# Optimization experiments

Measured on AMD Instinct MI355X. Metric: run time of the kernel, lower is better.

## Reference

```python
import jax, jax.numpy as jnp
import numpy as np

B, K, D = 4, 2048, 512
H, DQ, DV = 8, 64, 64
ATTN_SIZE = 128  # banded local window


def setup_inputs() -> dict:
    key = jax.random.key(0)
    ks = jax.random.split(key, 11)
    s = 1.0 / np.sqrt(D)
    so = 1.0 / np.sqrt(H * DV)
    return {
        "query": jax.random.normal(ks[0], (B, K, D), jnp.float32),
        "key": jax.random.normal(ks[1], (B, K, D), jnp.float32),
        "value": jax.random.normal(ks[2], (B, K, D), jnp.float32),
        "W_q": jax.random.uniform(ks[3], (H * DQ, D), jnp.float32, -s, s),
        "b_q": jax.random.uniform(ks[4], (H * DQ,), jnp.float32, -s, s),
        "W_k": jax.random.uniform(ks[5], (H * DQ, D), jnp.float32, -s, s),
        "b_k": jax.random.uniform(ks[6], (H * DQ,), jnp.float32, -s, s),
        "W_v": jax.random.uniform(ks[7], (H * DV, D), jnp.float32, -s, s),
        "b_v": jax.random.uniform(ks[8], (H * DV,), jnp.float32, -s, s),
        "W_o": jax.random.uniform(ks[9], (D, H * DV), jnp.float32, -so, so),
        "b_o": jax.random.uniform(ks[10], (D,), jnp.float32, -so, so),
    }


def reference(query, key, value, W_q, b_q, W_k, b_k, W_v, b_v, W_o, b_o):
    Klen = query.shape[1]
    # projections; chunk(h, -1) + cat(0) in torch == per-head split of last dim
    q = (query @ W_q.T + b_q).reshape(B, Klen, H, DQ)
    k = (key @ W_k.T + b_k).reshape(B, Klen, H, DQ)
    v = (value @ W_v.T + b_v).reshape(B, Klen, H, DV)
    # NOTE: original scales by sqrt(seq_len K), not sqrt(d_k)
    scores = jnp.einsum('bihq,bjhq->bhij', q, k) / jnp.sqrt(jnp.float32(Klen))
    i = jnp.arange(Klen)[:, None]
    j = jnp.arange(Klen)[None, :]
    # banded local mask (|i-j|<=attention_size) AND causal ('subsequent')
    allowed = (jnp.abs(i - j) <= ATTN_SIZE) & (j <= i)
    scores = jnp.where(allowed, scores, jnp.float32(-jnp.inf))
    probs = jax.nn.softmax(scores, axis=-1)
    attn = jnp.einsum('bhij,bjhv->bihv', probs, v).reshape(B, Klen, H * DV)
    return attn @ W_o.T + b_o
```

## Files before the change

### kernel.cpp

```cpp
#include <hip/hip_runtime.h>
#include <hip/hip_bf16.h>
#include <stdint.h>

#define B_ 4
#define K_ 2048
#define D_ 512
#define H_ 8
#define ATTN_ 128
#define M_ (B_ * K_)

typedef __attribute__((ext_vector_type(4))) float f32x4;
typedef __attribute__((ext_vector_type(8))) short bf16x8;
typedef __attribute__((ext_vector_type(8))) unsigned short u16x8;
typedef __attribute__((ext_vector_type(2))) unsigned int u32x2;

__device__ __forceinline__ unsigned short f2bf(float f) {
    union { float f; unsigned int i; } x; x.f = f;
    unsigned int r = x.i + 0x7fffu + ((x.i >> 16) & 1u);
    return (unsigned short)(r >> 16);
}
__device__ __forceinline__ float bf2f(unsigned short u) {
    union { unsigned int i; float f; } x; x.i = ((unsigned int)u) << 16; return x.f;
}
__device__ __forceinline__ void gload_lds16(const unsigned short* g, unsigned short* l) {
    __builtin_amdgcn_global_load_lds(
        (const __attribute__((address_space(1))) void*)g,
        (__attribute__((address_space(3))) void*)l, 16, 0, 0);
}
__device__ __forceinline__ unsigned lds_addr(const void* p) {
    return (unsigned)(unsigned long long)
        (const __attribute__((address_space(3))) void*)p;
}

struct Cvt { const float* s; unsigned short* d; int n8; };
struct CvtA { Cvt c[4]; };

__global__ __launch_bounds__(256)
void cvt_multi(CvtA a) {
    const Cvt c = a.c[blockIdx.y];
    const float4* s4 = (const float4*)c.s;
    u16x8* d8 = (u16x8*)c.d;
    for (int g = blockIdx.x * 256 + threadIdx.x; g < c.n8; g += gridDim.x * 256) {
        float4 f0 = s4[2 * g], f1 = s4[2 * g + 1];
        u16x8 o;
        o[0] = f2bf(f0.x); o[1] = f2bf(f0.y); o[2] = f2bf(f0.z); o[3] = f2bf(f0.w);
        o[4] = f2bf(f1.x); o[5] = f2bf(f1.y); o[6] = f2bf(f1.z); o[7] = f2bf(f1.w);
        d8[g] = o;
    }
}

struct QkvArgs {
    const float* A[3];
    const unsigned short* Wt[3];
    const float* bias[3];
    unsigned short* C[3];
};

__global__ __launch_bounds__(512, 4)
void gemm_qkv(QkvArgs args)
{
    __shared__ unsigned short As[2][128 * 64];
    __shared__ unsigned short Bs[2][128 * 64];

    const int z = blockIdx.y;
    const float* Az = args.A[z];
    const unsigned short* Wz = args.Wt[z];
    const float* biz = args.bias[z];
    unsigned short* Cz = args.C[z];

    const int id  = blockIdx.x;
    const int swz = (id & 7) * 32 + (id >> 3);
    const int bm  = (swz >> 2) * 128;
    const int bn  = (swz & 3) * 128;

    const int tid = threadIdx.x;
    const int w   = tid >> 6;
    const int l   = tid & 63;
    const int lr  = l & 15;
    const int lhi = l >> 4;
    const int wm  = (w >> 1) * 32;
    const int wn  = (w & 1) * 64;

    f32x4 acc[2][4];
    #pragma unroll
    for (int i = 0; i < 2; ++i)
        #pragma unroll
        for (int j = 0; j < 4; ++j) acc[i][j] = (f32x4){0.f, 0.f, 0.f, 0.f};

    float4 fa[2][2];
    auto loadA = [&](int t) {
        const int k0 = t * 64;
        #pragma unroll
        for (int it = 0; it < 2; ++it) {
            const int cid = it * 512 + tid;
            const int r = cid >> 3;
            const int c = (cid & 7) ^ (r & 7);
            const float* src = Az + (size_t)(bm + r) * D_ + k0 + c * 8;
            fa[it][0] = *(const float4*)src;
            fa[it][1] = *(const float4*)(src + 4);
        }
    };
    auto writeA = [&](int buf) {
        #pragma unroll
        for (int it = 0; it < 2; ++it) {
            const int cid = it * 512 + tid;
            u16x8 o;
            o[0] = f2bf(fa[it][0].x); o[1] = f2bf(fa[it][0].y);
            o[2] = f2bf(fa[it][0].z); o[3] = f2bf(fa[it][0].w);
            o[4] = f2bf(fa[it][1].x); o[5] = f2bf(fa[it][1].y);
            o[6] = f2bf(fa[it][1].z); o[7] = f2bf(fa[it][1].w);
            *(u16x8*)&As[buf][cid * 8] = o;
        }
    };
    auto stageB = [&](int buf, int t) {
        const int k0 = t * 64;
        #pragma unroll
        for (int it = 0; it < 2; ++it) {
            const int f  = it * 64 + l;
            const int r  = w * 16 + (f >> 3);
            const int cs = (f & 7) ^ (r & 7);
            gload_lds16(Wz + (size_t)(bn + r) * D_ + k0 + cs * 8,
                        &Bs[buf][(w * 128 + it * 64) * 8]);
        }
    };

    loadA(0); writeA(0);
    stageB(0, 0);
    __syncthreads();

    int buf = 0;
    for (int t = 0; t < 8; ++t) {
        if (t < 7) { loadA(t + 1); stageB(buf ^ 1, t + 1); }
        #pragma unroll
        for (int kk = 0; kk < 2; ++kk) {
            bf16x8 af[2], bfr[4];
            #pragma unroll
            for (int fm = 0; fm < 2; ++fm) {
                const int row = wm + fm * 16 + lr;
                const int ch  = (kk * 4 + lhi) ^ (lr & 7);
                af[fm] = *(const bf16x8*)&As[buf][row * 64 + ch * 8];
            }
            #pragma unroll
            for (int fn = 0; fn < 4; ++fn) {
                const int row = wn + fn * 16 + lr;
                const int ch  = (kk * 4 + lhi) ^ (lr & 7);
                bfr[fn] = *(const bf16x8*)&Bs[buf][row * 64 + ch * 8];
            }
            #pragma unroll
            for (int fm = 0; fm < 2; ++fm)
                #pragma unroll
                for (int fn = 0; fn < 4; ++fn)
                    acc[fm][fn] = __builtin_amdgcn_mfma_f32_16x16x32_bf16(
                        af[fm], bfr[fn], acc[fm][fn], 0, 0, 0);
        }
        if (t < 7) writeA(buf ^ 1);
        __syncthreads();
        buf ^= 1;
    }

    float bv[4];
    #pragma unroll
    for (int fn = 0; fn < 4; ++fn) bv[fn] = biz[bn + wn + fn * 16 + lr];

    #pragma unroll
    for (int fm = 0; fm < 2; ++fm)
        #pragma unroll
        for (int fn = 0; fn < 4; ++fn)
            #pragma unroll
            for (int rr = 0; rr < 4; ++rr) {
                const int row = bm + wm + fm * 16 + lhi * 4 + rr;
                const int col = bn + wn + fn * 16 + lr;
                Cz[(size_t)row * 512 + col] = f2bf(acc[fm][fn][rr] + bv[fn]);
            }
}

template<bool OUT_BF16>
__global__ __launch_bounds__(512)
void gemm_bf16k(const unsigned short* __restrict__ A,
                const unsigned short* __restrict__ W,
                const float* __restrict__ bias,
                void* __restrict__ C)
{
    __shared__ unsigned short As[2][128 * 64];
    __shared__ unsigned short Bs[2][128 * 64];

    const int id  = blockIdx.x;
    const int swz = (id & 7) * 32 + (id >> 3);
    const int bm  = (swz & 63) * 128;
    const int bn  = (swz >> 6) * 128;

    const int tid = threadIdx.x;
    const int w   = tid >> 6;
    const int l   = tid & 63;
    const int lr  = l & 15;
    const int lhi = l >> 4;
    const int wm  = (w >> 1) * 32;
    const int wn  = (w & 1) * 64;

    f32x4 acc[2][4];
    #pragma unroll
    for (int i = 0; i < 2; ++i)
        #pragma unroll
        for (int j = 0; j < 4; ++j) acc[i][j] = (f32x4){0.f, 0.f, 0.f, 0.f};

    auto stage = [&](int buf, int t) {
        const int k0 = t * 64;
        #pragma unroll
        for (int it = 0; it < 2; ++it) {
            const int f  = it * 64 + l;
            const int r  = w * 16 + (f >> 3);
            const int cs = (f & 7) ^ (r & 7);
            gload_lds16(A + (size_t)(bm + r) * D_ + k0 + cs * 8,
                        &As[buf][(w * 128 + it * 64) * 8]);
        }
        #pragma unroll
        for (int it = 0; it < 2; ++it) {
            const int f  = it * 64 + l;
            const int r  = w * 16 + (f >> 3);
            const int cs = (f & 7) ^ (r & 7);
            gload_lds16(W + (size_t)(bn + r) * D_ + k0 + cs * 8,
                        &Bs[buf][(w * 128 + it * 64) * 8]);
        }
    };

    stage(0, 0);
    __syncthreads();

    int buf = 0;
    for (int t = 0; t < 8; ++t) {
        if (t < 7) stage(buf ^ 1, t + 1);
        #pragma unroll
        for (int kk = 0; kk < 2; ++kk) {
            bf16x8 af[2], bfr[4];
            #pragma unroll
            for (int fm = 0; fm < 2; ++fm) {
                const int row = wm + fm * 16 + lr;
                const int ch  = (kk * 4 + lhi) ^ (lr & 7);
                af[fm] = *(const bf16x8*)&As[buf][row * 64 + ch * 8];
            }
            #pragma unroll
            for (int fn = 0; fn < 4; ++fn) {
                const int row = wn + fn * 16 + lr;
                const int ch  = (kk * 4 + lhi) ^ (lr & 7);
                bfr[fn] = *(const bf16x8*)&Bs[buf][row * 64 + ch * 8];
            }
            #pragma unroll
            for (int fm = 0; fm < 2; ++fm)
                #pragma unroll
                for (int fn = 0; fn < 4; ++fn)
                    acc[fm][fn] = __builtin_amdgcn_mfma_f32_16x16x32_bf16(
                        af[fm], bfr[fn], acc[fm][fn], 0, 0, 0);
        }
        __syncthreads();
        buf ^= 1;
    }

    float bv[4];
    #pragma unroll
    for (int fn = 0; fn < 4; ++fn) bv[fn] = bias[bn + wn + fn * 16 + lr];

    #pragma unroll
    for (int fm = 0; fm < 2; ++fm)
        #pragma unroll
        for (int fn = 0; fn < 4; ++fn)
            #pragma unroll
            for (int rr = 0; rr < 4; ++rr) {
                const int row = bm + wm + fm * 16 + lhi * 4 + rr;
                const int col = bn + wn + fn * 16 + lr;
                const float val = acc[fm][fn][rr] + bv[fn];
                if (OUT_BF16)
                    ((unsigned short*)C)[(size_t)row * 512 + col] = f2bf(val);
                else
                    ((float*)C)[(size_t)row * 512 + col] = val;
            }
}

__global__ __launch_bounds__(256)
void attn_mfma(const unsigned short* __restrict__ qb,
               const unsigned short* __restrict__ kb,
               const unsigned short* __restrict__ vb,
               unsigned short* __restrict__ ob)
{
    __shared__ unsigned short Ksh[192 * 64];
    __shared__ unsigned short Vsh[4 * 192 * 16];
    __shared__ unsigned short Psh[4 * 16 * 200];

    const int flat = blockIdx.x + 32 * (blockIdx.y + 8 * blockIdx.z);
    const int lg   = (flat & 7) * 128 + (flat >> 3);
    const int tile = lg & 31;
    const int h    = (lg >> 5) & 7;
    const int b    = lg >> 8;

    const int i0 = tile * 64;
    const int j0 = i0 - 128;
    const int tid = threadIdx.x;
    const int w   = tid >> 6;
    const int l   = tid & 63;
    const int lr  = l & 15;
    const int lhi = l >> 4;
    const float scale = 0.0220970869120796f;

    const size_t hbase = ((size_t)b * K_) * 512 + (size_t)h * 64;
    const unsigned short* kh = kb + hbase;
    const unsigned short* vh = vb + hbase;
    const unsigned short* qh = qb + hbase;
    unsigned short* oh = ob + hbase;

    #pragma unroll
    for (int it = 0; it < 6; ++it) {
        const int cg  = it * 4 + w;
        const int cid = cg * 64 + l;
        const int r = cid >> 3, c = cid & 7;
        const int cs = c ^ (r & 7);
        int j = j0 + r; if (j < 0) j = 0;
        gload_lds16(kh + (size_t)j * 512 + cs * 8, &Ksh[cg * 64 * 8]);
    }
    #pragma unroll
    for (int it = 0; it < 6; ++it) {
        const int cg  = it * 4 + w;
        const int cid = cg * 64 + l;
        const int blk = cid / 384;
        const int rem = cid - blk * 384;
        const int prow = rem >> 1, hf = rem & 1;
        const int a = prow >> 2, bb = prow & 3;
        const int k = (a < 24) ? (8 * a + bb) : (8 * (a - 24) + 4 + bb);
        int j = j0 + k; if (j < 0) j = 0;
        gload_lds16(vh + (size_t)j * 512 + blk * 16 + hf * 8, &Vsh[cg * 64 * 8]);
    }

    bf16x8 qa[2];
    {
        const unsigned short* qrow = qh + (size_t)(i0 + 16 * w + lr) * 512;
        qa[0] = *(const bf16x8*)(qrow + lhi * 8);
        qa[1] = *(const bf16x8*)(qrow + 32 + lhi * 8);
    }
    __syncthreads();

    const int jcbase = w & ~1;
    f32x4 sacc[10];
    #pragma unroll
    for (int jc = 0; jc < 10; ++jc) sacc[jc] = (f32x4){0.f, 0.f, 0.f, 0.f};

    __builtin_amdgcn_s_setprio(1);
    #pragma unroll
    for (int kk = 0; kk < 2; ++kk) {
        const int ch = (kk * 4 + lhi) ^ (lr & 7);
        #pragma unroll
        for (int jc = 0; jc < 10; ++jc) {
            const int row = (jcbase + jc) * 16 + lr;
            bf16x8 kf = *(const bf16x8*)&Ksh[row * 64 + ch * 8];
            sacc[jc] = __builtin_amdgcn_mfma_f32_16x16x32_bf16(
                qa[kk], kf, sacc[jc], 0, 0, 0);
        }
    }
    __builtin_amdgcn_s_setprio(0);

    unsigned short* myP = &Psh[w * 3200];
    const int lo0 = 128 - i0;
    float lsum[4] = {0.f, 0.f, 0.f, 0.f};
    #pragma unroll
    for (int jc = 0; jc < 10; ++jc) {
        const int jcol = (jcbase + jc) * 16 + lr;
        #pragma unroll
        for (int rr = 0; rr < 4; ++rr) {
            const int iloc = 16 * w + 4 * lhi + rr;
            const bool ok = (jcol >= iloc) && (jcol <= iloc + ATTN_) && (jcol >= lo0);
            const float p = ok ? __expf(fminf(sacc[jc][rr] * scale, 80.f)) : 0.f;
            lsum[rr] += p;
            myP[(4 * lhi + rr) * 200 + jcol] = f2bf(p);
        }
    }
    #pragma unroll
    for (int rr = 0; rr < 4; ++rr) {
        float s = lsum[rr];
        s += __shfl_xor(s, 1, 16);
        s += __shfl_xor(s, 2, 16);
        s += __shfl_xor(s, 4, 16);
        s += __shfl_xor(s, 8, 16);
        lsum[rr] = s;
    }

    const int kcbase = w >> 1;
    f32x4 oacc[4];
    #pragma unroll
    for (int fn = 0; fn < 4; ++fn) oacc[fn] = (f32x4){0.f, 0.f, 0.f, 0.f};
    const unsigned vbase = lds_addr(&Vsh[0]) + (unsigned)(l * 8);

    for (int kc5 = 0; kc5 < 5; ++kc5) {
        const int kc = kcbase + kc5;
        bf16x8 pa = *(const bf16x8*)&myP[lr * 200 + kc * 32 + lhi * 8];
        u32x2 vlo[4], vhi[4];
        #pragma unroll
        for (int fn = 0; fn < 4; ++fn) {
            const unsigned addr = vbase + (unsigned)((fn * 3072 + kc * 256) * 2);
            asm volatile("ds_read_b64_tr_b16 %0, %1" : "=v"(vlo[fn]) : "v"(addr));
            asm volatile("ds_read_b64_tr_b16 %0, %1 offset:3072"
                         : "=v"(vhi[fn]) : "v"(addr));
        }
        asm volatile("s_waitcnt lgkmcnt(0)" ::: "memory");
        __builtin_amdgcn_sched_barrier(0);
        __builtin_amdgcn_s_setprio(1);
        #pragma unroll
        for (int fn = 0; fn < 4; ++fn) {
            union { u32x2 h[2]; bf16x8 v; } u;
            u.h[0] = vlo[fn]; u.h[1] = vhi[fn];
            oacc[fn] = __builtin_amdgcn_mfma_f32_16x16x32_bf16(
                pa, u.v, oacc[fn], 0, 0, 0);
        }
        __builtin_amdgcn_s_setprio(0);
    }

    float inv[4];
    #pragma unroll
    for (int rr = 0; rr < 4; ++rr) inv[rr] = 1.f / lsum[rr];
    #pragma unroll
    for (int fn = 0; fn < 4; ++fn)
        #pragma unroll
        for (int rr = 0; rr < 4; ++rr) {
            const int row = i0 + 16 * w + 4 * lhi + rr;
            oh[(size_t)row * 512 + fn * 16 + lr] = f2bf(oacc[fn][rr] * inv[rr]);
        }
}

extern "C" void kernel_launch(void* const* d_in, const int* in_sizes, int n_in,
                              void* d_out, int out_size, void* d_ws, size_t ws_size,
                              hipStream_t stream)
{
    const float* query = (const float*)d_in[0];
    const float* key   = (const float*)d_in[1];
    const float* value = (const float*)d_in[2];
    const float* W_q   = (const float*)d_in[3];
    const float* b_q   = (const float*)d_in[4];
    const float* W_k   = (const float*)d_in[5];
    const float* b_k   = (const float*)d_in[6];
    const float* W_v   = (const float*)d_in[7];
    const float* b_v   = (const float*)d_in[8];
    const float* W_o   = (const float*)d_in[9];
    const float* b_o   = (const float*)d_in[10];
    float* out = (float*)d_out;

    const size_t NX = (size_t)M_ * 512;
    const size_t NW = 512 * 512;
    unsigned short* wqb = (unsigned short*)d_ws;
    unsigned short* wkb = wqb + NW;
    unsigned short* wvb = wkb + NW;
    unsigned short* wob = wvb + NW;
    unsigned short* qp  = wob + NW;
    unsigned short* kp  = qp + NX;
    unsigned short* vp  = kp + NX;
    unsigned short* ap  = vp + NX;

    const int NW8 = (int)(NW / 8);

    CvtA a;
    a.c[0] = { W_q, wqb, NW8 };
    a.c[1] = { W_k, wkb, NW8 };
    a.c[2] = { W_v, wvb, NW8 };
    a.c[3] = { W_o, wob, NW8 };
    cvt_multi<<<dim3(32, 4), 256, 0, stream>>>(a);

    QkvArgs qa;
    qa.A[0] = query; qa.A[1] = key; qa.A[2] = value;
    qa.Wt[0] = wqb;  qa.Wt[1] = wkb; qa.Wt[2] = wvb;
    qa.bias[0] = b_q; qa.bias[1] = b_k; qa.bias[2] = b_v;
    qa.C[0] = qp; qa.C[1] = kp; qa.C[2] = vp;
    gemm_qkv<<<dim3(256, 3), 512, 0, stream>>>(qa);

    attn_mfma<<<dim3(32, 8, 4), 256, 0, stream>>>(qp, kp, vp, ap);

    gemm_bf16k<false><<<256, 512, 0, stream>>>(ap, wob, b_o, out);
}
```

Measured before the change: 62.49 us.

## Restructure QKV projection to keep full-K weight slice in LDS and stream A from registers

The QKV GEMM tile changes from 128x128 with a double-buffered K loop to 256 rows by 64 columns. The whole 64x512 bf16 weight slice is loaded into LDS once, and the per-step LDS write of A is dropped. Each wave loads its fp32 A fragments straight from global memory into registers with a 3-deep prefetch, then converts them to bf16 with v_cvt_pk_bf16_f32 and feeds MFMA directly. This removes the per-iteration barriers and the A round trip through LDS. In exchange it uses more registers and 64KB of LDS per block, and the A global loads are less coalesced.

```diff
diff --git a/kernel.cpp b/kernel.cpp
--- a/kernel.cpp
+++ b/kernel.cpp
@@ -13,6 +13,7 @@
 typedef __attribute__((ext_vector_type(8))) short bf16x8;
 typedef __attribute__((ext_vector_type(8))) unsigned short u16x8;
 typedef __attribute__((ext_vector_type(2))) unsigned int u32x2;
+typedef __attribute__((ext_vector_type(4))) unsigned int u32x4;
 
 __device__ __forceinline__ unsigned short f2bf(float f) {
     union { float f; unsigned int i; } x; x.f = f;
@@ -21,6 +22,11 @@
 }
 __device__ __forceinline__ float bf2f(unsigned short u) {
     union { unsigned int i; float f; } x; x.i = ((unsigned int)u) << 16; return x.f;
+}
+__device__ __forceinline__ unsigned cvtpk(float lo, float hi) {
+    unsigned r;
+    asm("v_cvt_pk_bf16_f32 %0, %1, %2" : "=v"(r) : "v"(lo), "v"(hi));
+    return r;
 }
 __device__ __forceinline__ void gload_lds16(const unsigned short* g, unsigned short* l) {
     __builtin_amdgcn_global_load_lds(
@@ -49,7 +55,7 @@
     }
 }
 
-struct QkvArgs {
+struct PArgs {
     const float* A[3];
     const unsigned short* Wt[3];
     const float* bias[3];
@@ -57,110 +63,88 @@
 };
 
 __global__ __launch_bounds__(512, 4)
-void gemm_qkv(QkvArgs args)
+void gemm_qkv_persist(PArgs args)
 {
-    __shared__ unsigned short As[2][128 * 64];
-    __shared__ unsigned short Bs[2][128 * 64];
-
-    const int z = blockIdx.y;
+    __shared__ unsigned short Wl[64 * 512];
+
+    const int id = blockIdx.x;
+    const int nt = id / 96;
+    const int mg = id - nt * 96;
+    const int z  = mg >> 5;
+    const int bm = (mg & 31) * 256;
+    const int bn = nt * 64;
+
     const float* Az = args.A[z];
-    const unsigned short* Wz = args.Wt[z];
+    const unsigned short* Wz = args.Wt[z] + (size_t)bn * D_;
     const float* biz = args.bias[z];
     unsigned short* Cz = args.C[z];
-
-    const int id  = blockIdx.x;
-    const int swz = (id & 7) * 32 + (id >> 3);
-    const int bm  = (swz >> 2) * 128;
-    const int bn  = (swz & 3) * 128;
 
     const int tid = threadIdx.x;
     const int w   = tid >> 6;
     const int l   = tid & 63;
     const int lr  = l & 15;
     const int lhi = l >> 4;
-    const int wm  = (w >> 1) * 32;
-    const int wn  = (w & 1) * 64;
+    const int m0  = bm + w * 32;
 
     f32x4 acc[2][4];
     #pragma unroll
-    for (int i = 0; i < 2; ++i)
-        #pragma unroll
-        for (int j = 0; j < 4; ++j) acc[i][j] = (f32x4){0.f, 0.f, 0.f, 0.f};
-
-    float4 fa[2][2];
-    auto loadA = [&](int t) {
-        const int k0 = t * 64;
-        #pragma unroll
-        for (int it = 0; it < 2; ++it) {
-            const int cid = it * 512 + tid;
-            const int r = cid >> 3;
-            const int c = (cid & 7) ^ (r & 7);
-            const float* src = Az + (size_t)(bm + r) * D_ + k0 + c * 8;
-            fa[it][0] = *(const float4*)src;
-            fa[it][1] = *(const float4*)(src + 4);
+    for (int fm = 0; fm < 2; ++fm)
+        #pragma unroll
+        for (int fn = 0; fn < 4; ++fn) acc[fm][fn] = (f32x4){0.f, 0.f, 0.f, 0.f};
+
+    float4 fa[3][2][2];
+
+    auto loadA = [&](int kk, int s) {
+        #pragma unroll
+        for (int fm = 0; fm < 2; ++fm) {
+            const float* src = Az + (size_t)(m0 + fm * 16 + lr) * D_ + kk * 32 + lhi * 8;
+            fa[s][fm][0] = *(const float4*)src;
+            fa[s][fm][1] = *(const float4*)(src + 4);
         }
     };
-    auto writeA = [&](int buf) {
-        #pragma unroll
-        for (int it = 0; it < 2; ++it) {
-            const int cid = it * 512 + tid;
-            u16x8 o;
-            o[0] = f2bf(fa[it][0].x); o[1] = f2bf(fa[it][0].y);
-            o[2] = f2bf(fa[it][0].z); o[3] = f2bf(fa[it][0].w);
-            o[4] = f2bf(fa[it][1].x); o[5] = f2bf(fa[it][1].y);
-            o[6] = f2bf(fa[it][1].z); o[7] = f2bf(fa[it][1].w);
-            *(u16x8*)&As[buf][cid * 8] = o;
-        }
-    };
-    auto stageB = [&](int buf, int t) {
-        const int k0 = t * 64;
-        #pragma unroll
-        for (int it = 0; it < 2; ++it) {
-            const int f  = it * 64 + l;
-            const int r  = w * 16 + (f >> 3);
-            const int cs = (f & 7) ^ (r & 7);
-            gload_lds16(Wz + (size_t)(bn + r) * D_ + k0 + cs * 8,
-                        &Bs[buf][(w * 128 + it * 64) * 8]);
-        }
-    };
-
-    loadA(0); writeA(0);
-    stageB(0, 0);
+
+    loadA(0, 0); loadA(1, 1); loadA(2, 2);
+
+    #pragma unroll
+    for (int it = 0; it < 8; ++it) {
+        const int kc = it * 8 + w;
+        gload_lds16(Wz + (size_t)l * D_ + kc * 8, &Wl[kc * 512]);
+    }
     __syncthreads();
 
-    int buf = 0;
-    for (int t = 0; t < 8; ++t) {
-        if (t < 7) { loadA(t + 1); stageB(buf ^ 1, t + 1); }
-        #pragma unroll
-        for (int kk = 0; kk < 2; ++kk) {
-            bf16x8 af[2], bfr[4];
-            #pragma unroll
-            for (int fm = 0; fm < 2; ++fm) {
-                const int row = wm + fm * 16 + lr;
-                const int ch  = (kk * 4 + lhi) ^ (lr & 7);
-                af[fm] = *(const bf16x8*)&As[buf][row * 64 + ch * 8];
-            }
-            #pragma unroll
-            for (int fn = 0; fn < 4; ++fn) {
-                const int row = wn + fn * 16 + lr;
-                const int ch  = (kk * 4 + lhi) ^ (lr & 7);
-                bfr[fn] = *(const bf16x8*)&Bs[buf][row * 64 + ch * 8];
-            }
-            #pragma unroll
-            for (int fm = 0; fm < 2; ++fm)
-                #pragma unroll
-                for (int fn = 0; fn < 4; ++fn)
-                    acc[fm][fn] = __builtin_amdgcn_mfma_f32_16x16x32_bf16(
-                        af[fm], bfr[fn], acc[fm][fn], 0, 0, 0);
-        }
-        if (t < 7) writeA(buf ^ 1);
-        __syncthreads();
-        buf ^= 1;
+    #pragma unroll
+    for (int kk = 0; kk < 16; ++kk) {
+        const int s = kk % 3;
+
+        bf16x8 af[2];
+        #pragma unroll
+        for (int fm = 0; fm < 2; ++fm) {
+            const float4 f0 = fa[s][fm][0], f1 = fa[s][fm][1];
+            union { u32x4 u; bf16x8 b; } cv;
+            cv.u[0] = cvtpk(f0.x, f0.y);
+            cv.u[1] = cvtpk(f0.z, f0.w);
+            cv.u[2] = cvtpk(f1.x, f1.y);
+            cv.u[3] = cvtpk(f1.z, f1.w);
+            af[fm] = cv.b;
+        }
+        if (kk < 13) loadA(kk + 3, s);
+
+        bf16x8 bfr[4];
+        #pragma unroll
+        for (int fn = 0; fn < 4; ++fn)
+            bfr[fn] = *(const bf16x8*)&Wl[(kk * 4 + lhi) * 512 + (fn * 16 + lr) * 8];
+
+        #pragma unroll
+        for (int fm = 0; fm < 2; ++fm)
+            #pragma unroll
+            for (int fn = 0; fn < 4; ++fn)
+                acc[fm][fn] = __builtin_amdgcn_mfma_f32_16x16x32_bf16(
+                    af[fm], bfr[fn], acc[fm][fn], 0, 0, 0);
     }
 
     float bv[4];
     #pragma unroll
-    for (int fn = 0; fn < 4; ++fn) bv[fn] = biz[bn + wn + fn * 16 + lr];
+    for (int fn = 0; fn < 4; ++fn) bv[fn] = biz[bn + fn * 16 + lr];
 
     #pragma unroll
     for (int fm = 0; fm < 2; ++fm)
@@ -168,9 +152,9 @@
         for (int fn = 0; fn < 4; ++fn)
             #pragma unroll
             for (int rr = 0; rr < 4; ++rr) {
-                const int row = bm + wm + fm * 16 + lhi * 4 + rr;
-                const int col = bn + wn + fn * 16 + lr;
-                Cz[(size_t)row * 512 + col] = f2bf(acc[fm][fn][rr] + bv[fn]);
+                const int row = m0 + fm * 16 + lhi * 4 + rr;
+                const int col = bn + fn * 16 + lr;
+                Cz[(size_t)row * D_ + col] = f2bf(acc[fm][fn][rr] + bv[fn]);
             }
 }
 
@@ -459,12 +443,12 @@
     a.c[3] = { W_o, wob, NW8 };
     cvt_multi<<<dim3(32, 4), 256, 0, stream>>>(a);
 
-    QkvArgs qa;
+    PArgs qa;
     qa.A[0] = query; qa.A[1] = key; qa.A[2] = value;
     qa.Wt[0] = wqb;  qa.Wt[1] = wkb; qa.Wt[2] = wvb;
     qa.bias[0] = b_q; qa.bias[1] = b_k; qa.bias[2] = b_v;
     qa.C[0] = qp; qa.C[1] = kp; qa.C[2] = vp;
-    gemm_qkv<<<dim3(256, 3), 512, 0, stream>>>(qa);
+    gemm_qkv_persist<<<768, 512, 0, stream>>>(qa);
 
     attn_mfma<<<dim3(32, 8, 4), 256, 0, stream>>>(qp, kp, vp, ap);
 
```

Measured after the change: 91.04 us. +45.7%, slower.
